# Kernel tuning notes

Hardware: AMD Instinct MI355X
Metric: run time of the kernel (lower is better)

Reference implementation:

```python
import jax, jax.numpy as jnp
import numpy as np

K = 3  # kernel_size hard-coded in MorphologicalLoss
DICE_W, BOUND_W, MORPH_W = 0.3, 0.2, 0.2


def _kernel_mask():
    c = K // 2
    y, x = np.meshgrid(np.arange(K), np.arange(K), indexing='ij')
    m = ((x - c) ** 2 + (y - c) ** 2 <= c ** 2).astype(np.float32)  # circular (cross) SE
    return jnp.asarray(m.reshape(-1))  # [K*K]


def _patches(x):
    # x: [B,1,H,W] -> [B,1,K*K,H,W] (same as F.unfold with padding=K//2)
    p = K // 2
    xp = jnp.pad(x, ((0, 0), (0, 0), (p, p), (p, p)))
    H, W = x.shape[2], x.shape[3]
    views = [xp[:, :, dy:dy + H, dx:dx + W] for dy in range(K) for dx in range(K)]
    return jnp.stack(views, axis=2)


def _dilation(x, mask):
    m = mask.reshape(1, 1, -1, 1, 1)
    comp = (1.0 - _patches(x)) * m + (1.0 - m)
    return jnp.clip(1.0 - jnp.prod(comp, axis=2), 0.0, 1.0)


def _erosion(x, mask):
    m = mask.reshape(1, 1, -1, 1, 1)
    nb = _patches(x) * m + (1.0 - m)
    return jnp.clip(jnp.prod(nb, axis=2), 0.0, 1.0)


def _l1(a, b):
    return jnp.mean(jnp.abs(a - b))


def _loss(pred, target):
    mask = _kernel_mask()
    # reconstruction (l1)
    total = _l1(pred, target)
    # dice
    smooth = 1e-05
    inter = jnp.sum(pred * target)
    union = jnp.sum(pred) + jnp.sum(target)
    dice = jnp.clip((2.0 * inter + smooth) / (union + smooth), 0.0, 1.0)
    total = total + DICE_W * (-jnp.log(dice + 1e-08))
    # boundary gradients
    pgx = jnp.abs(pred[:, :, :, 1:] - pred[:, :, :, :-1])
    pgy = jnp.abs(pred[:, :, 1:, :] - pred[:, :, :-1, :])
    tgx = jnp.abs(target[:, :, :, 1:] - target[:, :, :, :-1])
    tgy = jnp.abs(target[:, :, 1:, :] - target[:, :, :-1, :])
    total = total + BOUND_W * 0.5 * (_l1(pgx, tgx) + _l1(pgy, tgy))
    # morphological consistency
    dil_loss = _l1(_dilation(pred, mask), _dilation(target, mask))
    ero_loss = _l1(_erosion(pred, mask), _erosion(target, mask))
    total = total + MORPH_W * 0.5 * (dil_loss + ero_loss)
    return jnp.maximum(total, 0.0)


def setup_inputs() -> dict:
    key = jax.random.key(0)
    k1, k2 = jax.random.split(key)
    B, C, H, W = 32, 1, 512, 512
    pred = jax.random.uniform(k1, (B, C, H, W), dtype=jnp.float32)
    target = jax.random.uniform(k2, (B, C, H, W), dtype=jnp.float32)
    return {"pred": pred, "target": target}


def reference(pred, target):
    return _loss(pred, target)
```

## Files before the change

kernel.cpp:

```cpp
#include <hip/hip_runtime.h>
#include <math.h>

constexpr int IMG_W  = 512;
constexpr int IMG_H  = 512;
constexpr int BATCH  = 32;
constexpr int NPIX   = BATCH * IMG_H * IMG_W;
constexpr int NROWS  = BATCH * IMG_H;
constexpr int RSTRIP = 16;
constexpr int NUNIT  = NROWS / RSTRIP;
constexpr int NTHR   = 256;
constexpr int NBLK   = NUNIT / 2;
constexpr int NXCD   = 8;
constexpr int NACC   = 8;

__global__ __launch_bounds__(NTHR) void morph_partials(
    const float* __restrict__ pred, const float* __restrict__ tgt,
    float* __restrict__ ws)
{
    float a[NACC];
#pragma unroll
    for (int k = 0; k < NACC; ++k) a[k] = 0.f;

    const int swz = (blockIdx.x % NXCD) * (NBLK / NXCD) + blockIdx.x / NXCD;

    const int unit    = swz * 2 + (threadIdx.x >> 7);
    const int lane128 = threadIdx.x & 127;
    const int lane64  = threadIdx.x & 63;
    const int g0      = unit * RSTRIP;
    const int img     = g0 >> 9;
    const int y0      = g0 & 511;
    const int imgbase = (img << 18) + (lane128 << 2);

    const float4 z4 = make_float4(0.f, 0.f, 0.f, 0.f);
    float4 pp, tp, pc, tc, pn, tn;

    if (y0 != 0) {
        const int idx = imgbase + ((y0 - 1) << 9);
        pp = *(const float4*)(pred + idx);
        tp = *(const float4*)(tgt  + idx);
    } else { pp = z4; tp = z4; }
    {
        const int idx = imgbase + (y0 << 9);
        pc = *(const float4*)(pred + idx);
        tc = *(const float4*)(tgt  + idx);
    }

    for (int r = 0; r < RSTRIP; ++r) {
        const int y = y0 + r;
        const bool hasD = (y != IMG_H - 1);
        if (hasD) {
            const int idx = imgbase + ((y + 1) << 9);
            pn = *(const float4*)(pred + idx);
            tn = *(const float4*)(tgt  + idx);
        } else { pn = z4; tn = z4; }

        float pl = __shfl_up(pc.w, 1, 64);
        float tl = __shfl_up(tc.w, 1, 64);
        float pr = __shfl_down(pc.x, 1, 64);
        float tr = __shfl_down(tc.x, 1, 64);
        const int i = imgbase + (y << 9);
        if (lane64 == 0) {
            if (lane128 == 0) { pl = 0.f; tl = 0.f; }
            else              { pl = pred[i - 1]; tl = tgt[i - 1]; }
        }
        if (lane64 == 63) {
            if (lane128 == 127) { pr = 0.f; tr = 0.f; }
            else                { pr = pred[i + 4]; tr = tgt[i + 4]; }
        }
        const bool hasR = (lane128 != 127);

        const float* pcA = &pc.x; const float* tcA = &tc.x;
        const float* ppA = &pp.x; const float* tpA = &tp.x;
        const float* pnA = &pn.x; const float* tnA = &tn.x;

#pragma unroll
        for (int j = 0; j < 4; ++j) {
            const float pcj = pcA[j], tcj = tcA[j];
            a[0] += fabsf(pcj - tcj);
            a[1] += pcj * tcj;
            a[2] += pcj;
            a[3] += tcj;
            if (j < 3)
                a[4] += fabsf(fabsf(pcA[j + 1] - pcj) - fabsf(tcA[j + 1] - tcj));
            const float plj = j ? pcA[j - 1] : pl;
            const float prj = (j < 3) ? pcA[j + 1] : pr;
            const float tlj = j ? tcA[j - 1] : tl;
            const float trj = (j < 3) ? tcA[j + 1] : tr;
            float dp = 1.f - (1.f - pcj) * (1.f - plj) * (1.f - prj) * (1.f - ppA[j]) * (1.f - pnA[j]);
            float dt = 1.f - (1.f - tcj) * (1.f - tlj) * (1.f - trj) * (1.f - tpA[j]) * (1.f - tnA[j]);
            dp = fminf(fmaxf(dp, 0.f), 1.f);
            dt = fminf(fmaxf(dt, 0.f), 1.f);
            a[6] += fabsf(dp - dt);
            float ep = pcj * plj * prj * ppA[j] * pnA[j];
            float et = tcj * tlj * trj * tpA[j] * tnA[j];
            ep = fminf(fmaxf(ep, 0.f), 1.f);
            et = fminf(fmaxf(et, 0.f), 1.f);
            a[7] += fabsf(ep - et);
        }
        if (hasR)
            a[4] += fabsf(fabsf(pr - pcA[3]) - fabsf(tr - tcA[3]));
        if (hasD) {
#pragma unroll
            for (int j = 0; j < 4; ++j)
                a[5] += fabsf(fabsf(pnA[j] - pcA[j]) - fabsf(tnA[j] - tcA[j]));
        }

        pp = pc; tp = tc; pc = pn; tc = tn;
    }

    __shared__ float sm[NACC][NTHR / 64];
#pragma unroll
    for (int k = 0; k < NACC; ++k) {
        float v = a[k];
        for (int o = 32; o > 0; o >>= 1) v += __shfl_down(v, o, 64);
        if ((threadIdx.x & 63) == 0) sm[k][threadIdx.x >> 6] = v;
    }
    __syncthreads();
    if (threadIdx.x < NACC) {
        float v = 0.f;
#pragma unroll
        for (int w = 0; w < NTHR / 64; ++w) v += sm[threadIdx.x][w];
        ws[threadIdx.x * NBLK + blockIdx.x] = v;
    }
}

__global__ __launch_bounds__(NTHR) void morph_final(
    const float* __restrict__ ws, float* __restrict__ out)
{
    __shared__ double sm[NACC][NTHR / 64];
#pragma unroll
    for (int k = 0; k < NACC; ++k) {
        double v = 0.0;
        for (int idx = threadIdx.x; idx < NBLK; idx += NTHR)
            v += (double)ws[k * NBLK + idx];
        for (int o = 32; o > 0; o >>= 1) v += __shfl_down(v, o, 64);
        if ((threadIdx.x & 63) == 0) sm[k][threadIdx.x >> 6] = v;
    }
    __syncthreads();
    if (threadIdx.x == 0) {
        double r[NACC];
#pragma unroll
        for (int k = 0; k < NACC; ++k) {
            double s = 0.0;
            for (int w = 0; w < NTHR / 64; ++w) s += sm[k][w];
            r[k] = s;
        }
        const double Npix  = (double)NPIX;
        const double Ngrad = (double)BATCH * IMG_H * (IMG_W - 1);

        double total = r[0] / Npix;
        double dice = (2.0 * r[1] + 1e-5) / (r[2] + r[3] + 1e-5);
        dice = fmin(fmax(dice, 0.0), 1.0);
        total += 0.3 * (-log(dice + 1e-8));
        total += 0.2 * 0.5 * ((r[4] + r[5]) / Ngrad);
        total += 0.2 * 0.5 * ((r[6] + r[7]) / Npix);

        out[0] = (float)fmax(total, 0.0);
    }
}

extern "C" void kernel_launch(void* const* d_in, const int* in_sizes, int n_in,
                              void* d_out, int out_size, void* d_ws, size_t ws_size,
                              hipStream_t stream) {
    const float* pred = (const float*)d_in[0];
    const float* tgt  = (const float*)d_in[1];
    float* out = (float*)d_out;
    float* ws  = (float*)d_ws;

    morph_partials<<<NBLK, NTHR, 0, stream>>>(pred, tgt, ws);
    morph_final<<<1, NTHR, 0, stream>>>(ws, out);
}
```

Baseline: 33.48 us.

## Share strip-boundary halo rows through LDS across four cooperating row strips

Each block now covers 64 consecutive rows with four 16-row strips. Strips are paired to walk toward or away from each other so that interior halo rows are exchanged through shared memory instead of being reloaded from global memory. Only the outer block edges still fetch halo rows from global memory. This cuts redundant halo loads, but it adds two block-wide barriers inside the loop, and the doubled block size may reduce scheduling flexibility.

```diff
diff --git a/kernel.cpp b/kernel.cpp
--- a/kernel.cpp
+++ b/kernel.cpp
@@ -6,12 +6,70 @@
 constexpr int BATCH  = 32;
 constexpr int NPIX   = BATCH * IMG_H * IMG_W;
 constexpr int NROWS  = BATCH * IMG_H;
-constexpr int RSTRIP = 16;
-constexpr int NUNIT  = NROWS / RSTRIP;
-constexpr int NTHR   = 256;
-constexpr int NBLK   = NUNIT / 2;
+constexpr int BROWS  = 64;
+constexpr int NTHR   = 512;
+constexpr int NBLK   = NROWS / BROWS;
 constexpr int NXCD   = 8;
 constexpr int NACC   = 8;
+
+__device__ __forceinline__ void row_compute(
+    const float4& pU, const float4& tU,
+    const float4& pC, const float4& tC,
+    const float4& pD, const float4& tD,
+    int gi, int lane128, int lane64, bool gyok,
+    const float* __restrict__ pred, const float* __restrict__ tgt,
+    float* a)
+{
+    float pl = __shfl_up(pC.w, 1, 64);
+    float tl = __shfl_up(tC.w, 1, 64);
+    float pr = __shfl_down(pC.x, 1, 64);
+    float tr = __shfl_down(tC.x, 1, 64);
+    if (lane64 == 0) {
+        if (lane128 == 0) { pl = 0.f; tl = 0.f; }
+        else              { pl = pred[gi - 1]; tl = tgt[gi - 1]; }
+    }
+    if (lane64 == 63) {
+        if (lane128 == 127) { pr = 0.f; tr = 0.f; }
+        else                { pr = pred[gi + 4]; tr = tgt[gi + 4]; }
+    }
+    const bool hasR = (lane128 != 127);
+
+    const float* pcA = &pC.x; const float* tcA = &tC.x;
+    const float* ppA = &pU.x; const float* tpA = &tU.x;
+    const float* pnA = &pD.x; const float* tnA = &tD.x;
+
+#pragma unroll
+    for (int j = 0; j < 4; ++j) {
+        const float pcj = pcA[j], tcj = tcA[j];
+        a[0] += fabsf(pcj - tcj);
+        a[1] += pcj * tcj;
+        a[2] += pcj;
+        a[3] += tcj;
+        if (j < 3)
+            a[4] += fabsf(fabsf(pcA[j + 1] - pcj) - fabsf(tcA[j + 1] - tcj));
+        const float plj = j ? pcA[j - 1] : pl;
+        const float prj = (j < 3) ? pcA[j + 1] : pr;
+        const float tlj = j ? tcA[j - 1] : tl;
+        const float trj = (j < 3) ? tcA[j + 1] : tr;
+        float dp = 1.f - (1.f - pcj) * (1.f - plj) * (1.f - prj) * (1.f - ppA[j]) * (1.f - pnA[j]);
+        float dt = 1.f - (1.f - tcj) * (1.f - tlj) * (1.f - trj) * (1.f - tpA[j]) * (1.f - tnA[j]);
+        dp = fminf(fmaxf(dp, 0.f), 1.f);
+        dt = fminf(fmaxf(dt, 0.f), 1.f);
+        a[6] += fabsf(dp - dt);
+        float ep = pcj * plj * prj * ppA[j] * pnA[j];
+        float et = tcj * tlj * trj * tpA[j] * tnA[j];
+        ep = fminf(fmaxf(ep, 0.f), 1.f);
+        et = fminf(fmaxf(et, 0.f), 1.f);
+        a[7] += fabsf(ep - et);
+    }
+    if (hasR)
+        a[4] += fabsf(fabsf(pr - pcA[3]) - fabsf(tr - tcA[3]));
+    if (gyok) {
+#pragma unroll
+        for (int j = 0; j < 4; ++j)
+            a[5] += fabsf(fabsf(pnA[j] - pcA[j]) - fabsf(tnA[j] - tcA[j]));
+    }
+}
 
 __global__ __launch_bounds__(NTHR) void morph_partials(
     const float* __restrict__ pred, const float* __restrict__ tgt,
@@ -23,115 +81,95 @@
 
     const int swz = (blockIdx.x % NXCD) * (NBLK / NXCD) + blockIdx.x / NXCD;
 
-    const int unit    = swz * 2 + (threadIdx.x >> 7);
+    const int unit    = threadIdx.x >> 7;
     const int lane128 = threadIdx.x & 127;
     const int lane64  = threadIdx.x & 63;
-    const int g0      = unit * RSTRIP;
-    const int img     = g0 >> 9;
-    const int y0      = g0 & 511;
+    const bool down   = !(unit & 1);
+    const int gb      = swz * BROWS;
+    const int img     = gb >> 9;
+    const int yb      = gb & 511;
     const int imgbase = (img << 18) + (lane128 << 2);
 
+    __shared__ float4 xch[4][2][128];
+    __shared__ float  smr[NACC][NTHR / 64];
+
     const float4 z4 = make_float4(0.f, 0.f, 0.f, 0.f);
-    float4 pp, tp, pc, tc, pn, tn;
-
-    if (y0 != 0) {
-        const int idx = imgbase + ((y0 - 1) << 9);
-        pp = *(const float4*)(pred + idx);
-        tp = *(const float4*)(tgt  + idx);
-    } else { pp = z4; tp = z4; }
+    float4 pU = z4, tU = z4, pC, tC, pD = z4, tD = z4;
+
+    const int yl0 = down ? unit * 16 : unit * 16 + 15;
     {
-        const int idx = imgbase + (y0 << 9);
-        pc = *(const float4*)(pred + idx);
-        tc = *(const float4*)(tgt  + idx);
-    }
-
-    for (int r = 0; r < RSTRIP; ++r) {
-        const int y = y0 + r;
-        const bool hasD = (y != IMG_H - 1);
-        if (hasD) {
-            const int idx = imgbase + ((y + 1) << 9);
-            pn = *(const float4*)(pred + idx);
-            tn = *(const float4*)(tgt  + idx);
-        } else { pn = z4; tn = z4; }
-
-        float pl = __shfl_up(pc.w, 1, 64);
-        float tl = __shfl_up(tc.w, 1, 64);
-        float pr = __shfl_down(pc.x, 1, 64);
-        float tr = __shfl_down(tc.x, 1, 64);
-        const int i = imgbase + (y << 9);
-        if (lane64 == 0) {
-            if (lane128 == 0) { pl = 0.f; tl = 0.f; }
-            else              { pl = pred[i - 1]; tl = tgt[i - 1]; }
-        }
-        if (lane64 == 63) {
-            if (lane128 == 127) { pr = 0.f; tr = 0.f; }
-            else                { pr = pred[i + 4]; tr = tgt[i + 4]; }
-        }
-        const bool hasR = (lane128 != 127);
-
-        const float* pcA = &pc.x; const float* tcA = &tc.x;
-        const float* ppA = &pp.x; const float* tpA = &tp.x;
-        const float* pnA = &pn.x; const float* tnA = &tn.x;
-
-#pragma unroll
-        for (int j = 0; j < 4; ++j) {
-            const float pcj = pcA[j], tcj = tcA[j];
-            a[0] += fabsf(pcj - tcj);
-            a[1] += pcj * tcj;
-            a[2] += pcj;
-            a[3] += tcj;
-            if (j < 3)
-                a[4] += fabsf(fabsf(pcA[j + 1] - pcj) - fabsf(tcA[j + 1] - tcj));
-            const float plj = j ? pcA[j - 1] : pl;
-            const float prj = (j < 3) ? pcA[j + 1] : pr;
-            const float tlj = j ? tcA[j - 1] : tl;
-            const float trj = (j < 3) ? tcA[j + 1] : tr;
-            float dp = 1.f - (1.f - pcj) * (1.f - plj) * (1.f - prj) * (1.f - ppA[j]) * (1.f - pnA[j]);
-            float dt = 1.f - (1.f - tcj) * (1.f - tlj) * (1.f - trj) * (1.f - tpA[j]) * (1.f - tnA[j]);
-            dp = fminf(fmaxf(dp, 0.f), 1.f);
-            dt = fminf(fmaxf(dt, 0.f), 1.f);
-            a[6] += fabsf(dp - dt);
-            float ep = pcj * plj * prj * ppA[j] * pnA[j];
-            float et = tcj * tlj * trj * tpA[j] * tnA[j];
-            ep = fminf(fmaxf(ep, 0.f), 1.f);
-            et = fminf(fmaxf(et, 0.f), 1.f);
-            a[7] += fabsf(ep - et);
-        }
-        if (hasR)
-            a[4] += fabsf(fabsf(pr - pcA[3]) - fabsf(tr - tcA[3]));
-        if (hasD) {
-#pragma unroll
-            for (int j = 0; j < 4; ++j)
-                a[5] += fabsf(fabsf(pnA[j] - pcA[j]) - fabsf(tnA[j] - tcA[j]));
-        }
-
-        pp = pc; tp = tc; pc = pn; tc = tn;
-    }
-
-    __shared__ float sm[NACC][NTHR / 64];
+        const int idx = imgbase + ((yb + yl0) << 9);
+        pC = *(const float4*)(pred + idx);
+        tC = *(const float4*)(tgt  + idx);
+    }
+    xch[unit][0][lane128] = pC;
+    xch[unit][1][lane128] = tC;
+    __syncthreads();
+    if (unit == 0) {
+        if (yb != 0) {
+            const int idx = imgbase + ((yb - 1) << 9);
+            pU = *(const float4*)(pred + idx);
+            tU = *(const float4*)(tgt  + idx);
+        }
+    } else if (unit == 1) {
+        pD = xch[2][0][lane128]; tD = xch[2][1][lane128];
+    } else if (unit == 2) {
+        pU = xch[1][0][lane128]; tU = xch[1][1][lane128];
+    } else {
+        if (yb != IMG_H - BROWS) {
+            const int idx = imgbase + ((yb + BROWS) << 9);
+            pD = *(const float4*)(pred + idx);
+            tD = *(const float4*)(tgt  + idx);
+        }
+    }
+
+    for (int r = 0; r < 16; ++r) {
+        const int yl = down ? unit * 16 + r : unit * 16 + 15 - r;
+        const int yi = yb + yl;
+        if (r == 15) {
+            __syncthreads();
+            xch[unit][0][lane128] = pC;
+            xch[unit][1][lane128] = tC;
+            __syncthreads();
+            const int pair = unit ^ 1;
+            if (down) { pD = xch[pair][0][lane128]; tD = xch[pair][1][lane128]; }
+            else      { pU = xch[pair][0][lane128]; tU = xch[pair][1][lane128]; }
+        } else {
+            const int ny  = down ? yi + 1 : yi - 1;
+            const int idx = imgbase + (ny << 9);
+            if (down) { pD = *(const float4*)(pred + idx); tD = *(const float4*)(tgt + idx); }
+            else      { pU = *(const float4*)(pred + idx); tU = *(const float4*)(tgt + idx); }
+        }
+        const bool gyok = (yi != IMG_H - 1);
+        const int  gi   = imgbase + (yi << 9);
+        row_compute(pU, tU, pC, tC, pD, tD, gi, lane128, lane64, gyok, pred, tgt, a);
+        if (down) { pU = pC; tU = tC; pC = pD; tC = tD; }
+        else      { pD = pC; tD = tC; pC = pU; tC = tU; }
+    }
+
 #pragma unroll
     for (int k = 0; k < NACC; ++k) {
         float v = a[k];
         for (int o = 32; o > 0; o >>= 1) v += __shfl_down(v, o, 64);
-        if ((threadIdx.x & 63) == 0) sm[k][threadIdx.x >> 6] = v;
+        if ((threadIdx.x & 63) == 0) smr[k][threadIdx.x >> 6] = v;
     }
     __syncthreads();
     if (threadIdx.x < NACC) {
         float v = 0.f;
 #pragma unroll
-        for (int w = 0; w < NTHR / 64; ++w) v += sm[threadIdx.x][w];
+        for (int w = 0; w < NTHR / 64; ++w) v += smr[threadIdx.x][w];
         ws[threadIdx.x * NBLK + blockIdx.x] = v;
     }
 }
 
-__global__ __launch_bounds__(NTHR) void morph_final(
+__global__ __launch_bounds__(256) void morph_final(
     const float* __restrict__ ws, float* __restrict__ out)
 {
-    __shared__ double sm[NACC][NTHR / 64];
+    __shared__ double sm[NACC][256 / 64];
 #pragma unroll
     for (int k = 0; k < NACC; ++k) {
         double v = 0.0;
-        for (int idx = threadIdx.x; idx < NBLK; idx += NTHR)
+        for (int idx = threadIdx.x; idx < NBLK; idx += 256)
             v += (double)ws[k * NBLK + idx];
         for (int o = 32; o > 0; o >>= 1) v += __shfl_down(v, o, 64);
         if ((threadIdx.x & 63) == 0) sm[k][threadIdx.x >> 6] = v;
@@ -142,7 +180,7 @@
 #pragma unroll
         for (int k = 0; k < NACC; ++k) {
             double s = 0.0;
-            for (int w = 0; w < NTHR / 64; ++w) s += sm[k][w];
+            for (int w = 0; w < 256 / 64; ++w) s += sm[k][w];
             r[k] = s;
         }
         const double Npix  = (double)NPIX;
@@ -168,5 +206,5 @@
     float* ws  = (float*)d_ws;
 
     morph_partials<<<NBLK, NTHR, 0, stream>>>(pred, tgt, ws);
-    morph_final<<<1, NTHR, 0, stream>>>(ws, out);
-}
+    morph_final<<<1, 256, 0, stream>>>(ws, out);
+}
```

New measurement: 29.90 us (median of 2 runs). 10.7% less time.
